# Kernel optimization log

Hardware: AMD Instinct MI355X
Metric: run time of the kernel (lower is better)

The kernel has to match this reference:

```python
import jax, jax.numpy as jnp
import numpy as np

B, T, C = 64, 512, 1024
D = C // 2  # split_len1 == split_len2
CLAMP = 5.0


def e(s):
    # exp(clamp * 0.636 * atan(s / clamp))
    return jnp.exp(CLAMP * 0.636 * jnp.arctan(s / CLAMP))


def gru_cell(x, h, Wih, Whh, bih, bhh):
    # Standard GRU cell, gate order (r, z, n) as in torch.nn.GRUCell.
    gi = x @ Wih.T + bih  # [B, 3D]
    gh = h @ Whh.T + bhh  # [B, 3D]
    i_r, i_z, i_n = gi[:, :D], gi[:, D:2 * D], gi[:, 2 * D:]
    h_r, h_z, h_n = gh[:, :D], gh[:, D:2 * D], gh[:, 2 * D:]
    r = jax.nn.sigmoid(i_r + h_r)
    z = jax.nn.sigmoid(i_z + h_z)
    n = jnp.tanh(i_n + r * h_n)
    return (1.0 - z) * n + z * h


def setup_inputs() -> dict:
    key = jax.random.key(0)
    ks = jax.random.split(key, 20)

    def p(k, shape, scale=0.05):
        return jax.random.normal(k, shape, jnp.float32) * scale

    inp = {"x": jax.random.normal(ks[0], (B, T, C), jnp.float32)}
    for i, name in enumerate(["s1", "s2"]):
        b = 1 + i * 6
        inp[f"{name}_Wih"] = p(ks[b], (3 * D, D))
        inp[f"{name}_Whh"] = p(ks[b + 1], (3 * D, D))
        inp[f"{name}_bih"] = p(ks[b + 2], (3 * D,))
        inp[f"{name}_bhh"] = p(ks[b + 3], (3 * D,))
        inp[f"{name}_Wo"] = p(ks[b + 4], (2 * D, D))
        inp[f"{name}_bo"] = p(ks[b + 5], (2 * D,))
    inp["cg1_W"] = p(ks[13], (D, D))
    inp["cg1_b"] = p(ks[14], (D,))
    inp["cg2_W"] = p(ks[15], (D, D))
    inp["cg2_b"] = p(ks[16], (D,))
    return inp


def reference(x, s1_Wih, s1_Whh, s1_bih, s1_bhh, s1_Wo, s1_bo,
              s2_Wih, s2_Whh, s2_bih, s2_bhh, s2_Wo, s2_bo,
              cg1_W, cg1_b, cg2_W, cg2_b):
    batch = x.shape[0]

    def step(carry, xt):
        h1, h2 = carry
        x1, x2 = xt[:, :D], xt[:, D:]
        # s2 GRU block on x2
        h2n = gru_cell(x2, h2, s2_Wih, s2_Whh, s2_bih, s2_bhh)
        r2 = h2n @ s2_Wo.T + s2_bo
        s2v, t2 = r2[:, :D], r2[:, D:]
        y1 = e(s2v) * x1 + t2
        # gate x2 with cg1 of OLD h1
        x2g = x2 * e(h1 @ cg1_W.T + cg1_b)
        # s1 GRU block on y1
        h1n = gru_cell(y1, h1, s1_Wih, s1_Whh, s1_bih, s1_bhh)
        r1 = h1n @ s1_Wo.T + s1_bo
        s1v, t1 = r1[:, :D], r1[:, D:]
        y2 = e(s1v) * x2g + t1
        # gate y1 with cg2 of OLD h2
        y1o = y1 * e(h2 @ cg2_W.T + cg2_b)
        return (h1n, h2n), jnp.concatenate([y1o, y2], axis=1)

    h0 = (jnp.zeros((batch, D), x.dtype), jnp.zeros((batch, D), x.dtype))
    _, ys = jax.lax.scan(step, h0, jnp.swapaxes(x, 0, 1))  # [T, B, C]
    return jnp.swapaxes(ys, 0, 1)  # [B, T, C]
```

## Files before the change

kernel.cpp:

```cpp
#include <hip/hip_runtime.h>
#include <math.h>

constexpr int kT = 512;
constexpr int kC = 1024;
constexpr int kD = 512;

typedef __attribute__((ext_vector_type(8))) short bf16x8;
typedef __attribute__((ext_vector_type(4))) float f32x4;
typedef __attribute__((ext_vector_type(4))) unsigned int u32x4;

__device__ __forceinline__ float b2f(unsigned short u) {
  unsigned int v = ((unsigned int)u) << 16;
  return __builtin_bit_cast(float, v);
}
__device__ __forceinline__ unsigned short f2b(float f) {
  unsigned int u = __builtin_bit_cast(unsigned int, f);
  u += 0x7fffu + ((u >> 16) & 1u);
  return (unsigned short)(u >> 16);
}
__device__ __forceinline__ float sigm(float x) {
  x = fminf(15.f, fmaxf(-15.f, x));
  return 1.f / (1.f + __expf(-x));
}
__device__ __forceinline__ float tanh_(float x) {
  x = fminf(15.f, fmaxf(-15.f, x));
  float e2 = __expf(2.f * x);
  return (e2 - 1.f) / (e2 + 1.f);
}
__device__ __forceinline__ float efun(float s) {
  return __expf((5.0f * 0.636f) * atanf(s * 0.2f));
}

__device__ __forceinline__ void st_b16_wt(unsigned short* p, unsigned short v) {
  asm volatile("global_store_short %0, %1, off sc0 sc1" ::"v"(p),
               "v"((unsigned int)v)
               : "memory");
}
__device__ __forceinline__ void st_f32_wt(float* p, float v) {
  asm volatile("global_store_dword %0, %1, off sc0 sc1" ::"v"(p), "v"(v)
               : "memory");
}

__device__ __forceinline__ unsigned int ldflag(const unsigned int* p) {
  return __hip_atomic_load(p, __ATOMIC_RELAXED, __HIP_MEMORY_SCOPE_AGENT);
}

__global__ __launch_bounds__(256) void cvt_x2_kernel(
    const float* __restrict__ x, unsigned short* __restrict__ xb2) {
  const int idx = blockIdx.x * 256 + threadIdx.x;
  const int e = idx * 8;
  const int dd = e & 511;
  const int tb = e >> 9;
  const int b = tb & 63;
  const int t = tb >> 6;
  const float* src = x + ((size_t)b * kT + t) * kC + kD + dd;
  f32x4 v0 = *(const f32x4*)src;
  f32x4 v1 = *(const f32x4*)(src + 4);
  bf16x8 o;
#pragma unroll
  for (int j = 0; j < 4; j++) {
    o[j] = (short)f2b(v0[j]);
    o[j + 4] = (short)f2b(v1[j]);
  }
  *(bf16x8*)(xb2 + e) = o;
}

__global__ __launch_bounds__(256, 1) void fused_glow_kernel(
    const float* __restrict__ x, const unsigned short* __restrict__ xb2,
    const float* __restrict__ A_Wih, const float* __restrict__ A_Whh,
    const float* __restrict__ A_bih, const float* __restrict__ A_bhh,
    const float* __restrict__ A_Wo, const float* __restrict__ A_bo,
    const float* __restrict__ A_cgW, const float* __restrict__ A_cgb,
    const float* __restrict__ B_Wih, const float* __restrict__ B_Whh,
    const float* __restrict__ B_bih, const float* __restrict__ B_bhh,
    const float* __restrict__ B_Wo, const float* __restrict__ B_bo,
    const float* __restrict__ B_cgW, const float* __restrict__ B_cgb,
    unsigned short* __restrict__ y1buf, float* __restrict__ out,
    unsigned short* __restrict__ hbA, unsigned short* __restrict__ hbB,
    unsigned int* __restrict__ flagsA, unsigned int* __restrict__ flagsB) {
  const int g = blockIdx.x;
  const bool isA = (g < 64);
  const int gl = isA ? g : (g - 64);
  const int tid = threadIdx.x;
  const int w = tid >> 6;
  const int l = tid & 63;
  const int q = l & 15;
  const int kg = l >> 4;
  const bool lo = (q < 8);
  const int qm = q & 7;
  const int d = 8 * gl + qm;
  const int browbase = 16 * w + 4 * kg;
  const int arow = 16 * w + q;
  const int acol = kg * 8;

  const float* Wih = isA ? A_Wih : B_Wih;
  const float* Whh = isA ? A_Whh : B_Whh;
  const float* bih = isA ? A_bih : B_bih;
  const float* bhh = isA ? A_bhh : B_bhh;
  const float* Wo = isA ? A_Wo : B_Wo;
  const float* bo = isA ? A_bo : B_bo;
  const float* cgW = isA ? A_cgW : B_cgW;
  const float* cgb = isA ? A_cgb : B_cgb;
  unsigned short* hbuf = isA ? hbA : hbB;
  unsigned int* myflag = (isA ? flagsA : flagsB) + (size_t)gl * 32;

  __shared__ __attribute__((aligned(16))) unsigned short wlds[80 * 512];
  for (int c = tid; c < 80 * 64; c += 256) {
    const int u = c >> 6, kb = c & 63;
    const int s8 = 8 * gl + (u & 7);
    const int sel = u >> 3;
    u32x4 v = {0u, 0u, 0u, 0u};
    if (sel < 9) {
      const float* wrp = (sel == 0)   ? Whh + (size_t)s8 * kD
                         : (sel == 1) ? Whh + (size_t)(512 + s8) * kD
                         : (sel == 2) ? Whh + (size_t)(1024 + s8) * kD
                         : (sel == 3) ? cgW + (size_t)s8 * kD
                         : (sel == 4) ? Wo + (size_t)s8 * kD
                         : (sel == 5) ? Wo + (size_t)(512 + s8) * kD
                         : (sel == 6) ? Wih + (size_t)s8 * kD
                         : (sel == 7) ? Wih + (size_t)(512 + s8) * kD
                                      : Wih + (size_t)(1024 + s8) * kD;
      const float* p = wrp + kb * 8;
#pragma unroll
      for (int j = 0; j < 4; j++)
        v[j] = (unsigned int)f2b(p[2 * j]) | ((unsigned int)f2b(p[2 * j + 1]) << 16);
    }
    const int byteoff = u * 1024 + ((kb * 16) ^ ((u & 15) << 4));
    *(u32x4*)((char*)wlds + byteoff) = v;
  }

  float biasv[5];
  biasv[0] = lo ? bhh[d] : bhh[512 + d];
  biasv[1] = lo ? bhh[1024 + d] : cgb[d];
  biasv[2] = lo ? bo[d] : bo[512 + d];
  biasv[3] = lo ? bih[d] : bih[512 + d];
  biasv[4] = lo ? bih[1024 + d] : 0.f;

  float hsl[4] = {0.f, 0.f, 0.f, 0.f};
  float ecp[4];
#pragma unroll
  for (int r = 0; r < 4; r++) ecp[r] = efun(cgb[d]);

  __syncthreads();

  const int sw = q << 4;
  const int s0 = isA ? 0 : 2;
  const int s1 = isA ? 512 : 514;
#pragma unroll 1
  for (int s = s0; s <= s1; ++s) {
    const int it = isA ? s : (s - 2);

    bf16x8 ax[16];
    float xopf[4] = {0.f, 0.f, 0.f, 0.f};
    if (isA) {
      const int itc = it < 511 ? it : 511;
      const unsigned short* xp = xb2 + ((size_t)itc * 64 + arow) * 512 + acol;
#pragma unroll
      for (int kk = 0; kk < 16; kk++) ax[kk] = *(const bf16x8*)(xp + kk * 32);
      if (lo) {
        const int ttc = s >= 1 ? s - 1 : 0;
#pragma unroll
        for (int r = 0; r < 4; r++)
          xopf[r] = x[(size_t)(browbase + r) * (kT * kC) + (size_t)ttc * kC + d];
      }
      if (s >= 1) {
        if (w == 0) {
          const unsigned int* fp = flagsA + (size_t)l * 32;
          unsigned int v = ldflag(fp);
          while (!__all((int)(v >= (unsigned)s))) {
            __builtin_amdgcn_s_sleep(1);
            v = ldflag(fp);
          }
        }
        __syncthreads();
      }
    } else {
      if (lo) {
        const int ttc = it >= 1 ? it - 1 : 0;
#pragma unroll
        for (int r = 0; r < 4; r++)
          xopf[r] =
              x[(size_t)(browbase + r) * (kT * kC) + (size_t)ttc * kC + kD + d];
      }
      const unsigned int tgtA = (unsigned)(s <= 513 ? s : 513);
      if (w == 0) {
        const unsigned int* fp = flagsA + (size_t)l * 32;
        unsigned int v = ldflag(fp);
        while (!__all((int)(v >= tgtA))) {
          __builtin_amdgcn_s_sleep(1);
          v = ldflag(fp);
        }
      }
      __syncthreads();
      const int ity = it < 511 ? it : 511;
      const unsigned short* yp = y1buf + ((size_t)ity * 64 + arow) * 512 + acol;
#pragma unroll
      for (int kk = 0; kk < 16; kk++) ax[kk] = *(const bf16x8*)(yp + kk * 32);
      if (s >= 3) {
        if (w == 0) {
          const unsigned int* fp = flagsB + (size_t)l * 32;
          unsigned int v = ldflag(fp);
          while (!__all((int)(v >= (unsigned)s))) {
            __builtin_amdgcn_s_sleep(1);
            v = ldflag(fp);
          }
        }
        __syncthreads();
      }
    }

    const unsigned short* hp =
        hbuf + (size_t)(isA ? s : it) * 32768 + (size_t)arow * 512 + acol;
    bf16x8 ah[16];
#pragma unroll
    for (int kk = 0; kk < 16; kk++) ah[kk] = *(const bf16x8*)(hp + kk * 32);

    f32x4 acc0 = {0.f, 0.f, 0.f, 0.f}, acc1 = {0.f, 0.f, 0.f, 0.f};
    f32x4 acc2 = {0.f, 0.f, 0.f, 0.f}, acc3 = {0.f, 0.f, 0.f, 0.f};
    f32x4 acc4 = {0.f, 0.f, 0.f, 0.f};
#pragma unroll
    for (int kk = 0; kk < 16; kk++) {
      const int kbyte = (kk * 32 + kg * 8) * 2;
      bf16x8 b0 = *(const bf16x8*)((const char*)wlds + q * 1024 + (kbyte ^ sw));
      bf16x8 b1 =
          *(const bf16x8*)((const char*)wlds + (16 + q) * 1024 + (kbyte ^ sw));
      bf16x8 b2 =
          *(const bf16x8*)((const char*)wlds + (32 + q) * 1024 + (kbyte ^ sw));
      bf16x8 b3 =
          *(const bf16x8*)((const char*)wlds + (48 + q) * 1024 + (kbyte ^ sw));
      bf16x8 b4 =
          *(const bf16x8*)((const char*)wlds + (64 + q) * 1024 + (kbyte ^ sw));
      acc0 = __builtin_amdgcn_mfma_f32_16x16x32_bf16(ah[kk], b0, acc0, 0, 0, 0);
      acc1 = __builtin_amdgcn_mfma_f32_16x16x32_bf16(ah[kk], b1, acc1, 0, 0, 0);
      acc2 = __builtin_amdgcn_mfma_f32_16x16x32_bf16(ah[kk], b2, acc2, 0, 0, 0);
      acc3 = __builtin_amdgcn_mfma_f32_16x16x32_bf16(ax[kk], b3, acc3, 0, 0, 0);
      acc4 = __builtin_amdgcn_mfma_f32_16x16x32_bf16(ax[kk], b4, acc4, 0, 0, 0);
    }
    float ab0[4], ab1[4], ab2[4], ab3[4], ab4[4];
#pragma unroll
    for (int r = 0; r < 4; r++) {
      ab0[r] = acc0[r] + biasv[0];
      ab1[r] = acc1[r] + biasv[1];
      ab2[r] = acc2[r] + biasv[2];
      ab3[r] = acc3[r] + biasv[3];
      ab4[r] = acc4[r] + biasv[4];
    }
    float ghz[4], tv[4], giz[4], ec_sh[4];
#pragma unroll
    for (int r = 0; r < 4; r++) {
      ghz[r] = __shfl_xor(ab0[r], 8, 64);
      tv[r] = __shfl_xor(ab2[r], 8, 64);
      giz[r] = __shfl_xor(ab3[r], 8, 64);
      ec_sh[r] = __shfl_xor(ecp[r], 8, 64);
    }
    const int tt = it - 1;
    if (lo) {
#pragma unroll
      for (int r = 0; r < 4; r++) {
        const int b = browbase + r;
        if (it >= 1) {
          const float es = efun(ab2[r]);
          float* op = out + (size_t)b * (kT * kC) + (size_t)tt * kC +
                      (isA ? 0 : kD) + d;
          if (isA) {
            const float yv = es * xopf[r] + tv[r];
            st_f32_wt(op, yv * ec_sh[r]);
            st_b16_wt(y1buf + ((size_t)tt * 64 + b) * 512 + d, f2b(yv));
          } else {
            st_f32_wt(op, es * (xopf[r] * ec_sh[r]) + tv[r]);
          }
        }
        if (it <= 511) {
          const float rr = sigm(ab3[r] + ab0[r]);
          const float zz = sigm(giz[r] + ghz[r]);
          const float nn = tanh_(ab4[r] + rr * ab1[r]);
          const float hn = (1.f - zz) * nn + zz * hsl[r];
          hsl[r] = hn;
          st_b16_wt(hbuf + (size_t)(it + 1) * 32768 + (size_t)b * 512 + d,
                    f2b(hn));
        }
      }
    } else {
#pragma unroll
      for (int r = 0; r < 4; r++) ecp[r] = efun(ab1[r]);
    }

    asm volatile("s_waitcnt vmcnt(0)" ::: "memory");
    __syncthreads();
    if (tid == 0)
      __hip_atomic_store(myflag, (unsigned)(s + 1), __ATOMIC_RELAXED,
                         __HIP_MEMORY_SCOPE_AGENT);
  }
}

extern "C" void kernel_launch(void* const* d_in, const int* in_sizes, int n_in,
                              void* d_out, int out_size, void* d_ws, size_t ws_size,
                              hipStream_t stream) {
  (void)in_sizes; (void)n_in; (void)out_size; (void)ws_size;
  const float* x = (const float*)d_in[0];
  const float* s1_Wih = (const float*)d_in[1];
  const float* s1_Whh = (const float*)d_in[2];
  const float* s1_bih = (const float*)d_in[3];
  const float* s1_bhh = (const float*)d_in[4];
  const float* s1_Wo = (const float*)d_in[5];
  const float* s1_bo = (const float*)d_in[6];
  const float* s2_Wih = (const float*)d_in[7];
  const float* s2_Whh = (const float*)d_in[8];
  const float* s2_bih = (const float*)d_in[9];
  const float* s2_bhh = (const float*)d_in[10];
  const float* s2_Wo = (const float*)d_in[11];
  const float* s2_bo = (const float*)d_in[12];
  const float* cg1_W = (const float*)d_in[13];
  const float* cg1_b = (const float*)d_in[14];
  const float* cg2_W = (const float*)d_in[15];
  const float* cg2_b = (const float*)d_in[16];
  float* out = (float*)d_out;
  char* ws = (char*)d_ws;

  unsigned short* xb2 = (unsigned short*)ws;
  unsigned short* y1b = (unsigned short*)(ws + 33554432);
  unsigned short* hbA = (unsigned short*)(ws + 67108864);
  unsigned short* hbB = (unsigned short*)(ws + 100728832);
  unsigned int* flagsA = (unsigned int*)(ws + 134348800);
  unsigned int* flagsB = (unsigned int*)(ws + 134348800 + 8192);

  hipMemsetAsync(ws + 67108864, 0, 65536, stream);
  hipMemsetAsync(ws + 100728832, 0, 65536, stream);
  hipMemsetAsync(ws + 134348800, 0, 16384, stream);

  cvt_x2_kernel<<<8192, 256, 0, stream>>>(x, xb2);

  fused_glow_kernel<<<128, 256, 0, stream>>>(
      x, xb2,
      s2_Wih, s2_Whh, s2_bih, s2_bhh, s2_Wo, s2_bo, cg2_W, cg2_b,
      s1_Wih, s1_Whh, s1_bih, s1_bhh, s1_Wo, s1_bo, cg1_W, cg1_b,
      y1b, out, hbA, hbB, flagsA, flagsB);
}
```

Baseline: 3.698 ms.

## Keep recurrent weight fragments in registers and defer output stores past flag signal

Loads the three recurrent-weight B fragments (bh0..bh2) into registers once before the time loop, so each step no longer re-reads them from LDS. Splits the step's MFMA work so the input-projection products run first and the recurrent-state products after. Moves the final output stores to after the flag release, taking them off the critical path, and widens the B-stage lag from two steps to three to relax the cross-block dependency. The change adds 48 bf16x8 live vector registers per thread, which risks register spills or lower occupancy, and it changes the pipeline skew between the two recurrent stages.

```diff
diff --git a/kernel.cpp b/kernel.cpp
--- a/kernel.cpp
+++ b/kernel.cpp
@@ -144,13 +144,23 @@
   __syncthreads();
 
   const int sw = q << 4;
-  const int s0 = isA ? 0 : 2;
-  const int s1 = isA ? 512 : 514;
+  bf16x8 bh0[16], bh1[16], bh2[16];
+#pragma unroll
+  for (int kk = 0; kk < 16; kk++) {
+    const int kbyte = (kk * 32 + kg * 8) * 2;
+    bh0[kk] = *(const bf16x8*)((const char*)wlds + q * 1024 + (kbyte ^ sw));
+    bh1[kk] = *(const bf16x8*)((const char*)wlds + (16 + q) * 1024 + (kbyte ^ sw));
+    bh2[kk] = *(const bf16x8*)((const char*)wlds + (32 + q) * 1024 + (kbyte ^ sw));
+  }
+
+  const int s0 = isA ? 0 : 3;
+  const int s1 = isA ? 512 : 515;
 #pragma unroll 1
   for (int s = s0; s <= s1; ++s) {
-    const int it = isA ? s : (s - 2);
+    const int it = isA ? s : (s - 3);
 
     bf16x8 ax[16];
+    bf16x8 ah[16];
     float xopf[4] = {0.f, 0.f, 0.f, 0.f};
     if (isA) {
       const int itc = it < 511 ? it : 511;
@@ -174,6 +184,10 @@
         }
         __syncthreads();
       }
+      const unsigned short* hp =
+          hbuf + (size_t)s * 32768 + (size_t)arow * 512 + acol;
+#pragma unroll
+      for (int kk = 0; kk < 16; kk++) ah[kk] = *(const bf16x8*)(hp + kk * 32);
     } else {
       if (lo) {
         const int ttc = it >= 1 ? it - 1 : 0;
@@ -182,7 +196,7 @@
           xopf[r] =
               x[(size_t)(browbase + r) * (kT * kC) + (size_t)ttc * kC + kD + d];
       }
-      const unsigned int tgtA = (unsigned)(s <= 513 ? s : 513);
+      const unsigned int tgtA = (unsigned)(s - 1 <= 513 ? s - 1 : 513);
       if (w == 0) {
         const unsigned int* fp = flagsA + (size_t)l * 32;
         unsigned int v = ldflag(fp);
@@ -196,7 +210,7 @@
       const unsigned short* yp = y1buf + ((size_t)ity * 64 + arow) * 512 + acol;
 #pragma unroll
       for (int kk = 0; kk < 16; kk++) ax[kk] = *(const bf16x8*)(yp + kk * 32);
-      if (s >= 3) {
+      if (s >= 4) {
         if (w == 0) {
           const unsigned int* fp = flagsB + (size_t)l * 32;
           unsigned int v = ldflag(fp);
@@ -207,35 +221,32 @@
         }
         __syncthreads();
       }
-    }
-
-    const unsigned short* hp =
-        hbuf + (size_t)(isA ? s : it) * 32768 + (size_t)arow * 512 + acol;
-    bf16x8 ah[16];
-#pragma unroll
-    for (int kk = 0; kk < 16; kk++) ah[kk] = *(const bf16x8*)(hp + kk * 32);
-
-    f32x4 acc0 = {0.f, 0.f, 0.f, 0.f}, acc1 = {0.f, 0.f, 0.f, 0.f};
-    f32x4 acc2 = {0.f, 0.f, 0.f, 0.f}, acc3 = {0.f, 0.f, 0.f, 0.f};
-    f32x4 acc4 = {0.f, 0.f, 0.f, 0.f};
+      const unsigned short* hp =
+          hbuf + (size_t)it * 32768 + (size_t)arow * 512 + acol;
+#pragma unroll
+      for (int kk = 0; kk < 16; kk++) ah[kk] = *(const bf16x8*)(hp + kk * 32);
+    }
+
+    f32x4 acc3 = {0.f, 0.f, 0.f, 0.f}, acc4 = {0.f, 0.f, 0.f, 0.f};
 #pragma unroll
     for (int kk = 0; kk < 16; kk++) {
       const int kbyte = (kk * 32 + kg * 8) * 2;
-      bf16x8 b0 = *(const bf16x8*)((const char*)wlds + q * 1024 + (kbyte ^ sw));
-      bf16x8 b1 =
-          *(const bf16x8*)((const char*)wlds + (16 + q) * 1024 + (kbyte ^ sw));
-      bf16x8 b2 =
-          *(const bf16x8*)((const char*)wlds + (32 + q) * 1024 + (kbyte ^ sw));
       bf16x8 b3 =
           *(const bf16x8*)((const char*)wlds + (48 + q) * 1024 + (kbyte ^ sw));
       bf16x8 b4 =
           *(const bf16x8*)((const char*)wlds + (64 + q) * 1024 + (kbyte ^ sw));
-      acc0 = __builtin_amdgcn_mfma_f32_16x16x32_bf16(ah[kk], b0, acc0, 0, 0, 0);
-      acc1 = __builtin_amdgcn_mfma_f32_16x16x32_bf16(ah[kk], b1, acc1, 0, 0, 0);
-      acc2 = __builtin_amdgcn_mfma_f32_16x16x32_bf16(ah[kk], b2, acc2, 0, 0, 0);
       acc3 = __builtin_amdgcn_mfma_f32_16x16x32_bf16(ax[kk], b3, acc3, 0, 0, 0);
       acc4 = __builtin_amdgcn_mfma_f32_16x16x32_bf16(ax[kk], b4, acc4, 0, 0, 0);
     }
+    f32x4 acc0 = {0.f, 0.f, 0.f, 0.f}, acc1 = {0.f, 0.f, 0.f, 0.f};
+    f32x4 acc2 = {0.f, 0.f, 0.f, 0.f};
+#pragma unroll
+    for (int kk = 0; kk < 16; kk++) {
+      acc0 = __builtin_amdgcn_mfma_f32_16x16x32_bf16(ah[kk], bh0[kk], acc0, 0, 0, 0);
+      acc1 = __builtin_amdgcn_mfma_f32_16x16x32_bf16(ah[kk], bh1[kk], acc1, 0, 0, 0);
+      acc2 = __builtin_amdgcn_mfma_f32_16x16x32_bf16(ah[kk], bh2[kk], acc2, 0, 0, 0);
+    }
+
     float ab0[4], ab1[4], ab2[4], ab3[4], ab4[4];
 #pragma unroll
     for (int r = 0; r < 4; r++) {
@@ -253,22 +264,19 @@
       giz[r] = __shfl_xor(ab3[r], 8, 64);
       ec_sh[r] = __shfl_xor(ecp[r], 8, 64);
     }
+
     const int tt = it - 1;
+    float yvs[4];
+    float esv[4];
     if (lo) {
 #pragma unroll
       for (int r = 0; r < 4; r++) {
         const int b = browbase + r;
-        if (it >= 1) {
-          const float es = efun(ab2[r]);
-          float* op = out + (size_t)b * (kT * kC) + (size_t)tt * kC +
-                      (isA ? 0 : kD) + d;
-          if (isA) {
-            const float yv = es * xopf[r] + tv[r];
-            st_f32_wt(op, yv * ec_sh[r]);
-            st_b16_wt(y1buf + ((size_t)tt * 64 + b) * 512 + d, f2b(yv));
-          } else {
-            st_f32_wt(op, es * (xopf[r] * ec_sh[r]) + tv[r]);
-          }
+        esv[r] = efun(ab2[r]);
+        if (isA && it >= 1) {
+          const float yv = esv[r] * xopf[r] + tv[r];
+          yvs[r] = yv;
+          st_b16_wt(y1buf + ((size_t)tt * 64 + b) * 512 + d, f2b(yv));
         }
         if (it <= 511) {
           const float rr = sigm(ab3[r] + ab0[r]);
@@ -290,6 +298,20 @@
     if (tid == 0)
       __hip_atomic_store(myflag, (unsigned)(s + 1), __ATOMIC_RELAXED,
                          __HIP_MEMORY_SCOPE_AGENT);
+
+    if (lo && it >= 1) {
+#pragma unroll
+      for (int r = 0; r < 4; r++) {
+        const int b = browbase + r;
+        float* op =
+            out + (size_t)b * (kT * kC) + (size_t)tt * kC + (isA ? 0 : kD) + d;
+        if (isA) {
+          st_f32_wt(op, yvs[r] * ec_sh[r]);
+        } else {
+          st_f32_wt(op, esv[r] * (xopf[r] * ec_sh[r]) + tv[r]);
+        }
+      }
+    }
   }
 }
 
```

Result: slower. 4.386 ms (+18.6%).

## Use per-wave per-step flags, fuse x2 bf16 conversion, defer output stores

Applied to the files above, without the earlier changes.

Replaces the block-wide flag plus __syncthreads handshake with per-wave flags indexed by step, so each wave signals and waits on its own row slice with no block barrier. It also removes the separate x2 conversion kernel by loading fp32 x and converting to bf16 inside the recurrence, and drops the memset of the h0 buffers by zero-filling registers at step 0. The flag is now published before the out stores so dependent blocks can proceed sooner. In exchange, the per-step x loads double in bytes, and the flag area is much larger and must be memset before each launch.

```diff
diff --git a/kernel.cpp b/kernel.cpp
--- a/kernel.cpp
+++ b/kernel.cpp
@@ -4,6 +4,7 @@
 constexpr int kT = 512;
 constexpr int kC = 1024;
 constexpr int kD = 512;
+constexpr int kFlagPlane = 516 * 64;
 
 typedef __attribute__((ext_vector_type(8))) short bf16x8;
 typedef __attribute__((ext_vector_type(4))) float f32x4;
@@ -40,33 +41,21 @@
   asm volatile("global_store_dword %0, %1, off sc0 sc1" ::"v"(p), "v"(v)
                : "memory");
 }
-
-__device__ __forceinline__ unsigned int ldflag(const unsigned int* p) {
-  return __hip_atomic_load(p, __ATOMIC_RELAXED, __HIP_MEMORY_SCOPE_AGENT);
-}
-
-__global__ __launch_bounds__(256) void cvt_x2_kernel(
-    const float* __restrict__ x, unsigned short* __restrict__ xb2) {
-  const int idx = blockIdx.x * 256 + threadIdx.x;
-  const int e = idx * 8;
-  const int dd = e & 511;
-  const int tb = e >> 9;
-  const int b = tb & 63;
-  const int t = tb >> 6;
-  const float* src = x + ((size_t)b * kT + t) * kC + kD + dd;
-  f32x4 v0 = *(const f32x4*)src;
-  f32x4 v1 = *(const f32x4*)(src + 4);
-  bf16x8 o;
-#pragma unroll
-  for (int j = 0; j < 4; j++) {
-    o[j] = (short)f2b(v0[j]);
-    o[j + 4] = (short)f2b(v1[j]);
-  }
-  *(bf16x8*)(xb2 + e) = o;
+__device__ __forceinline__ void st_u32_wt(unsigned int* p, unsigned int v) {
+  asm volatile("global_store_dword %0, %1, off sc0 sc1" ::"v"(p), "v"(v)
+               : "memory");
+}
+__device__ __forceinline__ unsigned int ld_u32_cc(const unsigned int* p) {
+  unsigned int r;
+  asm volatile("global_load_dword %0, %1, off sc0 sc1"
+               : "=v"(r)
+               : "v"(p)
+               : "memory");
+  return r;
 }
 
 __global__ __launch_bounds__(256, 1) void fused_glow_kernel(
-    const float* __restrict__ x, const unsigned short* __restrict__ xb2,
+    const float* __restrict__ x,
     const float* __restrict__ A_Wih, const float* __restrict__ A_Whh,
     const float* __restrict__ A_bih, const float* __restrict__ A_bhh,
     const float* __restrict__ A_Wo, const float* __restrict__ A_bo,
@@ -77,7 +66,7 @@
     const float* __restrict__ B_cgW, const float* __restrict__ B_cgb,
     unsigned short* __restrict__ y1buf, float* __restrict__ out,
     unsigned short* __restrict__ hbA, unsigned short* __restrict__ hbB,
-    unsigned int* __restrict__ flagsA, unsigned int* __restrict__ flagsB) {
+    unsigned int* __restrict__ flags) {
   const int g = blockIdx.x;
   const bool isA = (g < 64);
   const int gl = isA ? g : (g - 64);
@@ -102,7 +91,10 @@
   const float* cgW = isA ? A_cgW : B_cgW;
   const float* cgb = isA ? A_cgb : B_cgb;
   unsigned short* hbuf = isA ? hbA : hbB;
-  unsigned int* myflag = (isA ? flagsA : flagsB) + (size_t)gl * 32;
+
+  unsigned int* flgA = flags + (size_t)w * kFlagPlane;
+  unsigned int* flgB = flags + (size_t)(4 + w) * kFlagPlane;
+  unsigned int* flgSelf = isA ? flgA : flgB;
 
   __shared__ __attribute__((aligned(16))) unsigned short wlds[80 * 512];
   for (int c = tid; c < 80 * 64; c += 256) {
@@ -154,66 +146,77 @@
     float xopf[4] = {0.f, 0.f, 0.f, 0.f};
     if (isA) {
       const int itc = it < 511 ? it : 511;
-      const unsigned short* xp = xb2 + ((size_t)itc * 64 + arow) * 512 + acol;
-#pragma unroll
-      for (int kk = 0; kk < 16; kk++) ax[kk] = *(const bf16x8*)(xp + kk * 32);
+      const float* xp = x + ((size_t)arow * kT + itc) * kC + kD + acol;
+#pragma unroll
+      for (int kk = 0; kk < 16; kk++) {
+        f32x4 v0 = *(const f32x4*)(xp + kk * 32);
+        f32x4 v1 = *(const f32x4*)(xp + kk * 32 + 4);
+        bf16x8 t;
+#pragma unroll
+        for (int j = 0; j < 4; j++) {
+          t[j] = (short)f2b(v0[j]);
+          t[j + 4] = (short)f2b(v1[j]);
+        }
+        ax[kk] = t;
+      }
       if (lo) {
         const int ttc = s >= 1 ? s - 1 : 0;
 #pragma unroll
         for (int r = 0; r < 4; r++)
-          xopf[r] = x[(size_t)(browbase + r) * (kT * kC) + (size_t)ttc * kC + d];
+          xopf[r] = x[((size_t)(browbase + r) * kT + ttc) * kC + d];
       }
       if (s >= 1) {
-        if (w == 0) {
-          const unsigned int* fp = flagsA + (size_t)l * 32;
-          unsigned int v = ldflag(fp);
-          while (!__all((int)(v >= (unsigned)s))) {
-            __builtin_amdgcn_s_sleep(1);
-            v = ldflag(fp);
-          }
-        }
-        __syncthreads();
+        const unsigned int* fp = flgA + (size_t)(s - 1) * 64 + l;
+        unsigned int v = ld_u32_cc(fp);
+        while (!__all((int)(v == (unsigned)s))) {
+          __builtin_amdgcn_s_sleep(1);
+          v = ld_u32_cc(fp);
+        }
       }
     } else {
       if (lo) {
         const int ttc = it >= 1 ? it - 1 : 0;
 #pragma unroll
         for (int r = 0; r < 4; r++)
-          xopf[r] =
-              x[(size_t)(browbase + r) * (kT * kC) + (size_t)ttc * kC + kD + d];
-      }
-      const unsigned int tgtA = (unsigned)(s <= 513 ? s : 513);
-      if (w == 0) {
-        const unsigned int* fp = flagsA + (size_t)l * 32;
-        unsigned int v = ldflag(fp);
-        while (!__all((int)(v >= tgtA))) {
+          xopf[r] = x[((size_t)(browbase + r) * kT + ttc) * kC + kD + d];
+      }
+      {
+        const int ia = (s - 1) <= 512 ? (s - 1) : 512;
+        const unsigned int* fp = flgA + (size_t)ia * 64 + l;
+        unsigned int v = ld_u32_cc(fp);
+        while (!__all((int)(v == (unsigned)(ia + 1)))) {
           __builtin_amdgcn_s_sleep(1);
-          v = ldflag(fp);
-        }
-      }
-      __syncthreads();
+          v = ld_u32_cc(fp);
+        }
+      }
       const int ity = it < 511 ? it : 511;
       const unsigned short* yp = y1buf + ((size_t)ity * 64 + arow) * 512 + acol;
 #pragma unroll
       for (int kk = 0; kk < 16; kk++) ax[kk] = *(const bf16x8*)(yp + kk * 32);
       if (s >= 3) {
-        if (w == 0) {
-          const unsigned int* fp = flagsB + (size_t)l * 32;
-          unsigned int v = ldflag(fp);
-          while (!__all((int)(v >= (unsigned)s))) {
-            __builtin_amdgcn_s_sleep(1);
-            v = ldflag(fp);
-          }
-        }
-        __syncthreads();
-      }
-    }
-
-    const unsigned short* hp =
-        hbuf + (size_t)(isA ? s : it) * 32768 + (size_t)arow * 512 + acol;
+        const unsigned int* fp = flgB + (size_t)(s - 1) * 64 + l;
+        unsigned int v = ld_u32_cc(fp);
+        while (!__all((int)(v == (unsigned)s))) {
+          __builtin_amdgcn_s_sleep(1);
+          v = ld_u32_cc(fp);
+        }
+      }
+    }
+
+    const int hidx = isA ? s : it;
     bf16x8 ah[16];
-#pragma unroll
-    for (int kk = 0; kk < 16; kk++) ah[kk] = *(const bf16x8*)(hp + kk * 32);
+    if (hidx == 0) {
+#pragma unroll
+      for (int kk = 0; kk < 16; kk++) {
+#pragma unroll
+        for (int j = 0; j < 8; j++) ah[kk][j] = (short)0;
+      }
+    } else {
+      const unsigned short* hp =
+          hbuf + (size_t)hidx * 32768 + (size_t)arow * 512 + acol;
+#pragma unroll
+      for (int kk = 0; kk < 16; kk++) ah[kk] = *(const bf16x8*)(hp + kk * 32);
+    }
 
     f32x4 acc0 = {0.f, 0.f, 0.f, 0.f}, acc1 = {0.f, 0.f, 0.f, 0.f};
     f32x4 acc2 = {0.f, 0.f, 0.f, 0.f}, acc3 = {0.f, 0.f, 0.f, 0.f};
@@ -253,24 +256,14 @@
       giz[r] = __shfl_xor(ab3[r], 8, 64);
       ec_sh[r] = __shfl_xor(ecp[r], 8, 64);
     }
+
     const int tt = it - 1;
+    float yvs[4] = {0.f, 0.f, 0.f, 0.f};
     if (lo) {
-#pragma unroll
-      for (int r = 0; r < 4; r++) {
-        const int b = browbase + r;
-        if (it >= 1) {
-          const float es = efun(ab2[r]);
-          float* op = out + (size_t)b * (kT * kC) + (size_t)tt * kC +
-                      (isA ? 0 : kD) + d;
-          if (isA) {
-            const float yv = es * xopf[r] + tv[r];
-            st_f32_wt(op, yv * ec_sh[r]);
-            st_b16_wt(y1buf + ((size_t)tt * 64 + b) * 512 + d, f2b(yv));
-          } else {
-            st_f32_wt(op, es * (xopf[r] * ec_sh[r]) + tv[r]);
-          }
-        }
-        if (it <= 511) {
+      if (it <= 511) {
+#pragma unroll
+        for (int r = 0; r < 4; r++) {
+          const int b = browbase + r;
           const float rr = sigm(ab3[r] + ab0[r]);
           const float zz = sigm(giz[r] + ghz[r]);
           const float nn = tanh_(ab4[r] + rr * ab1[r]);
@@ -280,16 +273,37 @@
                     f2b(hn));
         }
       }
-    } else {
+      if (isA && it >= 1) {
+#pragma unroll
+        for (int r = 0; r < 4; r++) {
+          const int b = browbase + r;
+          yvs[r] = efun(ab2[r]) * xopf[r] + tv[r];
+          st_b16_wt(y1buf + ((size_t)tt * 64 + b) * 512 + d, f2b(yvs[r]));
+        }
+      }
+    }
+
+    asm volatile("s_waitcnt vmcnt(0)" ::: "memory");
+    if (l == 0)
+      st_u32_wt(flgSelf + (size_t)s * 64 + gl, (unsigned)(s + 1));
+
+    if (lo && it >= 1) {
+#pragma unroll
+      for (int r = 0; r < 4; r++) {
+        const int b = browbase + r;
+        float* op =
+            out + ((size_t)b * kT + tt) * kC + (isA ? 0 : kD) + d;
+        if (isA) {
+          st_f32_wt(op, yvs[r] * ec_sh[r]);
+        } else {
+          st_f32_wt(op, efun(ab2[r]) * (xopf[r] * ec_sh[r]) + tv[r]);
+        }
+      }
+    }
+    if (!lo) {
 #pragma unroll
       for (int r = 0; r < 4; r++) ecp[r] = efun(ab1[r]);
     }
-
-    asm volatile("s_waitcnt vmcnt(0)" ::: "memory");
-    __syncthreads();
-    if (tid == 0)
-      __hip_atomic_store(myflag, (unsigned)(s + 1), __ATOMIC_RELAXED,
-                         __HIP_MEMORY_SCOPE_AGENT);
   }
 }
 
@@ -317,22 +331,16 @@
   float* out = (float*)d_out;
   char* ws = (char*)d_ws;
 
-  unsigned short* xb2 = (unsigned short*)ws;
-  unsigned short* y1b = (unsigned short*)(ws + 33554432);
-  unsigned short* hbA = (unsigned short*)(ws + 67108864);
-  unsigned short* hbB = (unsigned short*)(ws + 100728832);
-  unsigned int* flagsA = (unsigned int*)(ws + 134348800);
-  unsigned int* flagsB = (unsigned int*)(ws + 134348800 + 8192);
-
-  hipMemsetAsync(ws + 67108864, 0, 65536, stream);
-  hipMemsetAsync(ws + 100728832, 0, 65536, stream);
-  hipMemsetAsync(ws + 134348800, 0, 16384, stream);
-
-  cvt_x2_kernel<<<8192, 256, 0, stream>>>(x, xb2);
+  unsigned short* y1b = (unsigned short*)ws;
+  unsigned short* hbA = (unsigned short*)(ws + 33554432);
+  unsigned short* hbB = (unsigned short*)(ws + 67174400);
+  unsigned int* flags = (unsigned int*)(ws + 100794368);
+
+  hipMemsetAsync(ws + 100794368, 0, 1056768, stream);
 
   fused_glow_kernel<<<128, 256, 0, stream>>>(
-      x, xb2,
+      x,
       s2_Wih, s2_Whh, s2_bih, s2_bhh, s2_Wo, s2_bo, cg2_W, cg2_b,
       s1_Wih, s1_Whh, s1_bih, s1_bhh, s1_Wo, s1_bo, cg1_W, cg1_b,
-      y1b, out, hbA, hbB, flagsA, flagsB);
-}
+      y1b, out, hbA, hbB, flags);
+}
```

Measured after the change: 5.551 ms. +50.1%, slower.
